# Kernel optimization log

Hardware: AMD Instinct MI355X
Metric: run time of the kernel (lower is better)

The kernel has to match this reference:

```python
import jax, jax.numpy as jnp
import numpy as np

KERNEL_MUL = 2.0
KERNEL_NUM = 5

def setup_inputs() -> dict:
    key = jax.random.key(0)
    k1, k2 = jax.random.split(key)
    source = jax.random.normal(k1, (4096, 256), dtype=jnp.float32)
    target = jax.random.normal(k2, (4096, 256), dtype=jnp.float32)
    return {"source": source, "target": target}

def reference(source, target):
    B = source.shape[0]
    total = jnp.concatenate([source, target], axis=0)           # [2N, D]
    n = total.shape[0]
    # pairwise squared L2 distances via expansion (same math as
    # ((total0 - total1)**2).sum(2) without the [2N,2N,D] intermediate)
    sq = jnp.sum(total * total, axis=-1)                         # [2N]
    l2 = jnp.maximum(sq[:, None] + sq[None, :] - 2.0 * (total @ total.T), 0.0)  # [2N,2N]
    # bandwidth from data mean of off-diagonal distances (detached in torch via .data)
    bandwidth = jax.lax.stop_gradient(jnp.sum(l2)) / (n * n - n)
    bandwidth = bandwidth / (KERNEL_MUL ** (KERNEL_NUM // 2))
    kernels = jnp.zeros_like(l2)
    for i in range(KERNEL_NUM):
        kernels = kernels + jnp.exp(-l2 / (bandwidth * (KERNEL_MUL ** i)))
    xx = kernels[:B, :B]
    yy = kernels[B:, B:]
    xy = kernels[:B, B:]
    yx = kernels[B:, :B]
    return jnp.mean(xx + yy - xy - yx)
```

## Files before the change

kernel.cpp:

```cpp
#include <hip/hip_runtime.h>


#define NROWS 8192
#define BHALF 4096
#define DDIM  256
#define TILE  128
#define NTILE 64
#define NBLK  2080

typedef __attribute__((ext_vector_type(8))) short bf16x8;
typedef __attribute__((ext_vector_type(4))) float f32x4;
typedef __attribute__((ext_vector_type(2))) float f32x2;
typedef __attribute__((ext_vector_type(4))) unsigned short u16x4;

struct Ws {
  float coef;
  float Spart[256];
  float cpart[256][256];
  float sq[NROWS];
  float part[NBLK];
};

__device__ __forceinline__ unsigned short f2bf(float x) {
  unsigned int u = __builtin_bit_cast(unsigned int, x);
  return (unsigned short)((u + 0x7fffu + ((u >> 16) & 1u)) >> 16);
}

__device__ __forceinline__ const float* row_ptr(const float* src, const float* tgt, int i) {
  return (i < BHALF) ? (src + (size_t)i * DDIM) : (tgt + (size_t)(i - BHALF) * DDIM);
}

__global__ __launch_bounds__(256) void k_prep(const float* __restrict__ src,
                                              const float* __restrict__ tgt,
                                              Ws* __restrict__ ws,
                                              unsigned short* __restrict__ tb,
                                              int conv) {
  __shared__ float cls[4][256];
  __shared__ float sred[4];
  int tid = threadIdx.x, wave = tid >> 6, lane = tid & 63;
  int row0 = blockIdx.x * 32 + wave * 8;
  float c0 = 0.f, c1 = 0.f, c2 = 0.f, c3 = 0.f;
  float s[8];
  #pragma unroll
  for (int r = 0; r < 8; ++r) {
    const float4* rp = (const float4*)row_ptr(src, tgt, row0 + r);
    float4 x = rp[lane];
    if (conv) {
      u16x4 b = { f2bf(x.x), f2bf(x.y), f2bf(x.z), f2bf(x.w) };
      int rg = row0 + r;
      int t = rg >> 7, rl = rg & 127;
      int cg = lane >> 1;
      int kc = cg >> 3, cwp = cg & 7;
      int slot = cwp ^ (rl & 7);
      *(u16x4*)&tb[((size_t)(t * 4 + kc) * 128 + rl) * 64 + slot * 8 + (lane & 1) * 4] = b;
    }
    c0 += x.x; c1 += x.y; c2 += x.z; c3 += x.w;
    s[r] = x.x * x.x + x.y * x.y + x.z * x.z + x.w * x.w;
  }
  #pragma unroll
  for (int off = 32; off > 0; off >>= 1) {
    #pragma unroll
    for (int r = 0; r < 8; ++r) s[r] += __shfl_xor(s[r], off);
  }
  if (lane == 0) {
    float Sw = 0.f;
    #pragma unroll
    for (int r = 0; r < 8; ++r) { ws->sq[row0 + r] = s[r]; Sw += s[r]; }
    sred[wave] = Sw;
  }
  cls[wave][lane * 4 + 0] = c0;
  cls[wave][lane * 4 + 1] = c1;
  cls[wave][lane * 4 + 2] = c2;
  cls[wave][lane * 4 + 3] = c3;
  __syncthreads();
  ws->cpart[blockIdx.x][tid] = cls[0][tid] + cls[1][tid] + cls[2][tid] + cls[3][tid];
  if (tid == 0) ws->Spart[blockIdx.x] = sred[0] + sred[1] + sred[2] + sred[3];
}

__global__ __launch_bounds__(256) void k_bw(Ws* __restrict__ ws) {
  __shared__ float redm[4], reds[4];
  int tid = threadIdx.x, wave = tid >> 6, lane = tid & 63;
  float mc = 0.f;
  for (int b0 = 0; b0 < 256; b0 += 16) {
    float v[16];
    #pragma unroll
    for (int j = 0; j < 16; ++j) v[j] = ws->cpart[b0 + j][tid];
    #pragma unroll
    for (int j = 0; j < 16; ++j) mc += v[j];
  }
  float p = mc * mc;
  float sp = ws->Spart[tid];
  #pragma unroll
  for (int off = 32; off > 0; off >>= 1) {
    p  += __shfl_xor(p, off);
    sp += __shfl_xor(sp, off);
  }
  if (lane == 0) { redm[wave] = p; reds[wave] = sp; }
  __syncthreads();
  if (tid == 0) {
    float msq = redm[0] + redm[1] + redm[2] + redm[3];
    float S   = reds[0] + reds[1] + reds[2] + reds[3];
    double n = (double)NROWS;
    double sum_l2 = 2.0 * n * (double)S - 2.0 * (double)msq;
    double bw = sum_l2 / (n * n - n) / 4.0;
    ws->coef = (float)(1.4426950408889634 / (16.0 * bw));
  }
}

__device__ __forceinline__ void stage_tiles(const unsigned short* gA,
                                            const unsigned short* gB,
                                            unsigned short* lA, unsigned short* lB,
                                            int kc) {
  #pragma unroll
  for (int t = 0; t < 4; ++t) {
    __builtin_amdgcn_global_load_lds(
        (const __attribute__((address_space(1))) void*)(gA + (size_t)kc * 8192 + t * 512),
        (__attribute__((address_space(3))) void*)(lA + t * 512), 16, 0, 0);
    __builtin_amdgcn_global_load_lds(
        (const __attribute__((address_space(1))) void*)(gB + (size_t)kc * 8192 + t * 512),
        (__attribute__((address_space(3))) void*)(lB + t * 512), 16, 0, 0);
  }
}

template <int FAST>
__global__ __launch_bounds__(256, 4) void k_main(const unsigned short* __restrict__ tb,
                                                 const float* __restrict__ src,
                                                 const float* __restrict__ tgt,
                                                 Ws* __restrict__ ws) {
  int bid = blockIdx.x;
  int idx = (bid & 7) * (NBLK / 8) + (bid >> 3);
  int ti = (int)((129.0 - sqrt(129.0 * 129.0 - 8.0 * (double)idx)) * 0.5);
  while (64 * (ti + 1) - ((ti + 1) * ti) / 2 <= idx) ++ti;
  while (64 * ti - (ti * (ti - 1)) / 2 > idx) --ti;
  int tj = ti + (idx - (64 * ti - (ti * (ti - 1)) / 2));

  __shared__ __align__(16) unsigned short As[TILE * 64];
  __shared__ __align__(16) unsigned short Bs[TILE * 64];
  __shared__ float wsum[4];

  int tid = threadIdx.x;
  int wave = tid >> 6, lane = tid & 63;
  int wm = wave >> 1, wn = wave & 1;
  int lr = lane & 15, q = lane >> 4;
  int Ib = ti * TILE, Jb = tj * TILE;

  f32x4 zero = {0.f, 0.f, 0.f, 0.f};
  f32x4 acc[4][4];
  #pragma unroll
  for (int m = 0; m < 4; ++m)
    #pragma unroll
    for (int n = 0; n < 4; ++n) acc[m][n] = zero;

  const unsigned short* gA = nullptr; const unsigned short* gB = nullptr;
  if (FAST) {
    gA = tb + (size_t)ti * 4 * 8192 + wave * 2048 + lane * 8;
    gB = tb + (size_t)tj * 4 * 8192 + wave * 2048 + lane * 8;
  }
  int r0 = tid >> 4, c4 = tid & 15;

  #pragma unroll
  for (int kc = 0; kc < 4; ++kc) {
    if (kc) __syncthreads();
    if (FAST) {
      stage_tiles(gA, gB, &As[(wave * 32) * 64], &Bs[(wave * 32) * 64], kc);
    } else {
      #pragma unroll
      for (int rr = 0; rr < 8; ++rr) {
        int row = rr * 16 + r0;
        int sw = ((c4 >> 1) ^ (row & 7)) * 8 + (c4 & 1) * 4;
        float4 va = ((const float4*)row_ptr(src, tgt, Ib + row))[kc * 16 + c4];
        u16x4 ba = { f2bf(va.x), f2bf(va.y), f2bf(va.z), f2bf(va.w) };
        *(u16x4*)&As[row * 64 + sw] = ba;
        float4 vb = ((const float4*)row_ptr(src, tgt, Jb + row))[kc * 16 + c4];
        u16x4 bb = { f2bf(vb.x), f2bf(vb.y), f2bf(vb.z), f2bf(vb.w) };
        *(u16x4*)&Bs[row * 64 + sw] = bb;
      }
    }
    __syncthreads();
    #pragma unroll
    for (int kk = 0; kk < 2; ++kk) {
      int cidx = ((kk * 4 + q) ^ (lr & 7)) << 3;
      bf16x8 af[4], bfr[4];
      #pragma unroll
      for (int m = 0; m < 4; ++m)
        af[m] = *(const bf16x8*)&As[(wm * 64 + m * 16 + lr) * 64 + cidx];
      #pragma unroll
      for (int n = 0; n < 4; ++n)
        bfr[n] = *(const bf16x8*)&Bs[(wn * 64 + n * 16 + lr) * 64 + cidx];
      #pragma unroll
      for (int m = 0; m < 4; ++m)
        #pragma unroll
        for (int n = 0; n < 4; ++n)
          acc[m][n] = __builtin_amdgcn_mfma_f32_16x16x32_bf16(af[m], bfr[n], acc[m][n], 0, 0, 0);
    }
  }

  float coef = ws->coef;
  float coef2 = 2.f * coef;
  int ibase = Ib + wm * 64;
  int jbase = Jb + wn * 64;
  float nscj[4];
  f32x2 nsci01[4], nsci23[4];
  #pragma unroll
  for (int n = 0; n < 4; ++n) nscj[n] = -ws->sq[jbase + n * 16 + lr] * coef;
  #pragma unroll
  for (int m = 0; m < 4; ++m) {
    nsci01[m] = f32x2{ -ws->sq[ibase + m * 16 + q * 4 + 0] * coef,
                       -ws->sq[ibase + m * 16 + q * 4 + 1] * coef };
    nsci23[m] = f32x2{ -ws->sq[ibase + m * 16 + q * 4 + 2] * coef,
                       -ws->sq[ibase + m * 16 + q * 4 + 3] * coef };
  }

  const f32x2 c2v = { coef2, coef2 };
  f32x2 accA = {0.f, 0.f}, accB = {0.f, 0.f};
  f32x2 accC = {0.f, 0.f}, accD = {0.f, 0.f};
  #pragma unroll
  for (int m = 0; m < 4; ++m) {
    #pragma unroll
    for (int n = 0; n < 4; ++n) {
      f32x4 g = acc[m][n];
      f32x2 bj = { nscj[n], nscj[n] };
      f32x2 b01 = nsci01[m] + bj;
      f32x2 b23 = nsci23[m] + bj;
      f32x2 a01 = f32x2{g[0], g[1]} * c2v + b01;
      f32x2 a23 = f32x2{g[2], g[3]} * c2v + b23;
      f32x2 t0, t1;
      t0.x = __builtin_amdgcn_exp2f(a01.x); t0.y = __builtin_amdgcn_exp2f(a01.y);
      t1.x = __builtin_amdgcn_exp2f(a23.x); t1.y = __builtin_amdgcn_exp2f(a23.y);
      f32x2 p0 = t0 * t0, p1 = t1 * t1;
      f32x2 q0 = p0 * p0, q1 = p1 * p1;
      f32x2 r0v = q0 * q0, r1v = q1 * q1;
      accA += t0 + p0;
      accB += q0 + r0v;
      accA = r0v * r0v + accA;
      accC += t1 + p1;
      accD += q1 + r1v;
      accC = r1v * r1v + accC;
    }
  }
  float lsum = (accA.x + accA.y) + (accB.x + accB.y)
             + (accC.x + accC.y) + (accD.x + accD.y);
  #pragma unroll
  for (int off = 32; off > 0; off >>= 1) lsum += __shfl_xor(lsum, off);
  if (lane == 0) wsum[wave] = lsum;
  __syncthreads();
  if (tid == 0) {
    float tot = wsum[0] + wsum[1] + wsum[2] + wsum[3];
    float sA = (ti < 32) ? 1.f : -1.f;
    float sB = (tj < 32) ? 1.f : -1.f;
    float fac = sA * sB * ((ti == tj) ? 1.f : 2.f);
    ws->part[blockIdx.x] = fac * tot;
  }
}

__global__ __launch_bounds__(256) void k_final(const Ws* __restrict__ ws,
                                               float* __restrict__ out) {
  __shared__ double red[4];
  int tid = threadIdx.x, wave = tid >> 6, lane = tid & 63;
  double s = 0.0;
  for (int i = tid; i < NBLK; i += 256) s += (double)ws->part[i];
  #pragma unroll
  for (int off = 32; off > 0; off >>= 1) s += __shfl_xor(s, off);
  if (lane == 0) red[wave] = s;
  __syncthreads();
  if (tid == 0)
    out[0] = (float)((red[0] + red[1] + red[2] + red[3]) /
                     ((double)BHALF * (double)BHALF));
}

extern "C" void kernel_launch(void* const* d_in, const int* in_sizes, int n_in,
                              void* d_out, int out_size, void* d_ws, size_t ws_size,
                              hipStream_t stream) {
  const float* src = (const float*)d_in[0];
  const float* tgt = (const float*)d_in[1];
  Ws* ws = (Ws*)d_ws;
  float* out = (float*)d_out;

  size_t wsoff = (sizeof(Ws) + 255) & ~(size_t)255;
  size_t need = wsoff + (size_t)NROWS * DDIM * 2;
  bool fast = ws_size >= need;
  unsigned short* tb = fast ? (unsigned short*)((char*)d_ws + wsoff) : nullptr;

  hipLaunchKernelGGL(k_prep, dim3(256), dim3(256), 0, stream, src, tgt, ws, tb,
                     fast ? 1 : 0);
  hipLaunchKernelGGL(k_bw, dim3(1), dim3(256), 0, stream, ws);
  if (fast)
    hipLaunchKernelGGL((k_main<1>), dim3(NBLK), dim3(256), 0, stream, tb, src, tgt, ws);
  else
    hipLaunchKernelGGL((k_main<0>), dim3(NBLK), dim3(256), 0, stream, tb, src, tgt, ws);
  hipLaunchKernelGGL(k_final, dim3(1), dim3(256), 0, stream, ws, out);
}
```

Before: 100.0 us.

## Make k_main persistent over multiple tiles and prefetch next tile during epilogue

```diff
diff --git a/kernel.cpp b/kernel.cpp
--- a/kernel.cpp
+++ b/kernel.cpp
@@ -7,6 +7,7 @@
 #define TILE  128
 #define NTILE 64
 #define NBLK  2080
+#define NPER  1024
 
 typedef __attribute__((ext_vector_type(8))) short bf16x8;
 typedef __attribute__((ext_vector_type(4))) float f32x4;
@@ -28,6 +29,14 @@
 
 __device__ __forceinline__ const float* row_ptr(const float* src, const float* tgt, int i) {
   return (i < BHALF) ? (src + (size_t)i * DDIM) : (tgt + (size_t)(i - BHALF) * DDIM);
+}
+
+__device__ __forceinline__ void derive_tile(int idx, int& ti_o, int& tj_o) {
+  int t = (int)((129.0 - sqrt(129.0 * 129.0 - 8.0 * (double)idx)) * 0.5);
+  while (64 * (t + 1) - ((t + 1) * t) / 2 <= idx) ++t;
+  while (64 * t - (t * (t - 1)) / 2 > idx) --t;
+  ti_o = t;
+  tj_o = t + (idx - (64 * t - (t * (t - 1)) / 2));
 }
 
 __global__ __launch_bounds__(256) void k_prep(const float* __restrict__ src,
@@ -127,12 +136,10 @@
                                                  const float* __restrict__ src,
                                                  const float* __restrict__ tgt,
                                                  Ws* __restrict__ ws) {
-  int bid = blockIdx.x;
-  int idx = (bid & 7) * (NBLK / 8) + (bid >> 3);
-  int ti = (int)((129.0 - sqrt(129.0 * 129.0 - 8.0 * (double)idx)) * 0.5);
-  while (64 * (ti + 1) - ((ti + 1) * ti) / 2 <= idx) ++ti;
-  while (64 * ti - (ti * (ti - 1)) / 2 > idx) --ti;
-  int tj = ti + (idx - (64 * ti - (ti * (ti - 1)) / 2));
+  int b = blockIdx.x;
+  int c = b & 7, p = b >> 3;
+  int nw = (p < 4) ? 3 : 2;
+  int idx = c * 260 + p;
 
   __shared__ __align__(16) unsigned short As[TILE * 64];
   __shared__ __align__(16) unsigned short Bs[TILE * 64];
@@ -142,114 +149,161 @@
   int wave = tid >> 6, lane = tid & 63;
   int wm = wave >> 1, wn = wave & 1;
   int lr = lane & 15, q = lane >> 4;
-  int Ib = ti * TILE, Jb = tj * TILE;
-
-  f32x4 zero = {0.f, 0.f, 0.f, 0.f};
-  f32x4 acc[4][4];
-  #pragma unroll
-  for (int m = 0; m < 4; ++m)
-    #pragma unroll
-    for (int n = 0; n < 4; ++n) acc[m][n] = zero;
-
+
+  int ti, tj;
+  derive_tile(idx, ti, tj);
+
+  unsigned short* lA = &As[(wave * 32) * 64];
+  unsigned short* lB = &Bs[(wave * 32) * 64];
   const unsigned short* gA = nullptr; const unsigned short* gB = nullptr;
   if (FAST) {
-    gA = tb + (size_t)ti * 4 * 8192 + wave * 2048 + lane * 8;
-    gB = tb + (size_t)tj * 4 * 8192 + wave * 2048 + lane * 8;
+    gA = tb + (size_t)ti * 32768 + wave * 2048 + lane * 8;
+    gB = tb + (size_t)tj * 32768 + wave * 2048 + lane * 8;
+    stage_tiles(gA, gB, lA, lB, 0);
   }
   int r0 = tid >> 4, c4 = tid & 15;
-
-  #pragma unroll
-  for (int kc = 0; kc < 4; ++kc) {
-    if (kc) __syncthreads();
-    if (FAST) {
-      stage_tiles(gA, gB, &As[(wave * 32) * 64], &Bs[(wave * 32) * 64], kc);
-    } else {
-      #pragma unroll
-      for (int rr = 0; rr < 8; ++rr) {
-        int row = rr * 16 + r0;
-        int sw = ((c4 >> 1) ^ (row & 7)) * 8 + (c4 & 1) * 4;
-        float4 va = ((const float4*)row_ptr(src, tgt, Ib + row))[kc * 16 + c4];
-        u16x4 ba = { f2bf(va.x), f2bf(va.y), f2bf(va.z), f2bf(va.w) };
-        *(u16x4*)&As[row * 64 + sw] = ba;
-        float4 vb = ((const float4*)row_ptr(src, tgt, Jb + row))[kc * 16 + c4];
-        u16x4 bb = { f2bf(vb.x), f2bf(vb.y), f2bf(vb.z), f2bf(vb.w) };
-        *(u16x4*)&Bs[row * 64 + sw] = bb;
-      }
-    }
-    __syncthreads();
-    #pragma unroll
-    for (int kk = 0; kk < 2; ++kk) {
-      int cidx = ((kk * 4 + q) ^ (lr & 7)) << 3;
-      bf16x8 af[4], bfr[4];
-      #pragma unroll
-      for (int m = 0; m < 4; ++m)
-        af[m] = *(const bf16x8*)&As[(wm * 64 + m * 16 + lr) * 64 + cidx];
-      #pragma unroll
-      for (int n = 0; n < 4; ++n)
-        bfr[n] = *(const bf16x8*)&Bs[(wn * 64 + n * 16 + lr) * 64 + cidx];
-      #pragma unroll
-      for (int m = 0; m < 4; ++m)
-        #pragma unroll
-        for (int n = 0; n < 4; ++n)
-          acc[m][n] = __builtin_amdgcn_mfma_f32_16x16x32_bf16(af[m], bfr[n], acc[m][n], 0, 0, 0);
-    }
-  }
-
   float coef = ws->coef;
   float coef2 = 2.f * coef;
-  int ibase = Ib + wm * 64;
-  int jbase = Jb + wn * 64;
-  float nscj[4];
-  f32x2 nsci01[4], nsci23[4];
-  #pragma unroll
-  for (int n = 0; n < 4; ++n) nscj[n] = -ws->sq[jbase + n * 16 + lr] * coef;
-  #pragma unroll
-  for (int m = 0; m < 4; ++m) {
-    nsci01[m] = f32x2{ -ws->sq[ibase + m * 16 + q * 4 + 0] * coef,
-                       -ws->sq[ibase + m * 16 + q * 4 + 1] * coef };
-    nsci23[m] = f32x2{ -ws->sq[ibase + m * 16 + q * 4 + 2] * coef,
-                       -ws->sq[ibase + m * 16 + q * 4 + 3] * coef };
-  }
-
   const f32x2 c2v = { coef2, coef2 };
-  f32x2 accA = {0.f, 0.f}, accB = {0.f, 0.f};
-  f32x2 accC = {0.f, 0.f}, accD = {0.f, 0.f};
-  #pragma unroll
-  for (int m = 0; m < 4; ++m) {
-    #pragma unroll
-    for (int n = 0; n < 4; ++n) {
-      f32x4 g = acc[m][n];
-      f32x2 bj = { nscj[n], nscj[n] };
-      f32x2 b01 = nsci01[m] + bj;
-      f32x2 b23 = nsci23[m] + bj;
-      f32x2 a01 = f32x2{g[0], g[1]} * c2v + b01;
-      f32x2 a23 = f32x2{g[2], g[3]} * c2v + b23;
-      f32x2 t0, t1;
-      t0.x = __builtin_amdgcn_exp2f(a01.x); t0.y = __builtin_amdgcn_exp2f(a01.y);
-      t1.x = __builtin_amdgcn_exp2f(a23.x); t1.y = __builtin_amdgcn_exp2f(a23.y);
-      f32x2 p0 = t0 * t0, p1 = t1 * t1;
-      f32x2 q0 = p0 * p0, q1 = p1 * p1;
-      f32x2 r0v = q0 * q0, r1v = q1 * q1;
-      accA += t0 + p0;
-      accB += q0 + r0v;
-      accA = r0v * r0v + accA;
-      accC += t1 + p1;
-      accD += q1 + r1v;
-      accC = r1v * r1v + accC;
-    }
-  }
-  float lsum = (accA.x + accA.y) + (accB.x + accB.y)
-             + (accC.x + accC.y) + (accD.x + accD.y);
-  #pragma unroll
-  for (int off = 32; off > 0; off >>= 1) lsum += __shfl_xor(lsum, off);
-  if (lane == 0) wsum[wave] = lsum;
-  __syncthreads();
-  if (tid == 0) {
-    float tot = wsum[0] + wsum[1] + wsum[2] + wsum[3];
-    float sA = (ti < 32) ? 1.f : -1.f;
-    float sB = (tj < 32) ? 1.f : -1.f;
-    float fac = sA * sB * ((ti == tj) ? 1.f : 2.f);
-    ws->part[blockIdx.x] = fac * tot;
+  const int coffbase = 0;
+  (void)coffbase;
+
+  for (int w = 0; w < nw; ++w) {
+    f32x4 zero = {0.f, 0.f, 0.f, 0.f};
+    f32x4 acc[4][4];
+    #pragma unroll
+    for (int m = 0; m < 4; ++m)
+      #pragma unroll
+      for (int n = 0; n < 4; ++n) acc[m][n] = zero;
+
+    if (FAST) {
+      if (w == 0) __syncthreads();
+      #pragma unroll
+      for (int kc = 0; kc < 4; ++kc) {
+        if (kc) {
+          __syncthreads();
+          stage_tiles(gA, gB, lA, lB, kc);
+          __syncthreads();
+        }
+        #pragma unroll
+        for (int kk = 0; kk < 2; ++kk) {
+          int cidx = ((kk * 4 + q) ^ (lr & 7)) << 3;
+          bf16x8 af[4], bfr[4];
+          #pragma unroll
+          for (int m = 0; m < 4; ++m)
+            af[m] = *(const bf16x8*)&As[(wm * 64 + m * 16 + lr) * 64 + cidx];
+          #pragma unroll
+          for (int n = 0; n < 4; ++n)
+            bfr[n] = *(const bf16x8*)&Bs[(wn * 64 + n * 16 + lr) * 64 + cidx];
+          #pragma unroll
+          for (int m = 0; m < 4; ++m)
+            #pragma unroll
+            for (int n = 0; n < 4; ++n)
+              acc[m][n] = __builtin_amdgcn_mfma_f32_16x16x32_bf16(af[m], bfr[n], acc[m][n], 0, 0, 0);
+        }
+      }
+      __syncthreads();
+    } else {
+      int Ib = ti * TILE, Jb = tj * TILE;
+      #pragma unroll
+      for (int kc = 0; kc < 4; ++kc) {
+        if (kc || w) __syncthreads();
+        #pragma unroll
+        for (int rr = 0; rr < 8; ++rr) {
+          int row = rr * 16 + r0;
+          int sw = ((c4 >> 1) ^ (row & 7)) * 8 + (c4 & 1) * 4;
+          float4 va = ((const float4*)row_ptr(src, tgt, Ib + row))[kc * 16 + c4];
+          u16x4 ba = { f2bf(va.x), f2bf(va.y), f2bf(va.z), f2bf(va.w) };
+          *(u16x4*)&As[row * 64 + sw] = ba;
+          float4 vb = ((const float4*)row_ptr(src, tgt, Jb + row))[kc * 16 + c4];
+          u16x4 bb = { f2bf(vb.x), f2bf(vb.y), f2bf(vb.z), f2bf(vb.w) };
+          *(u16x4*)&Bs[row * 64 + sw] = bb;
+        }
+        __syncthreads();
+        #pragma unroll
+        for (int kk = 0; kk < 2; ++kk) {
+          int cidx = ((kk * 4 + q) ^ (lr & 7)) << 3;
+          bf16x8 af[4], bfr[4];
+          #pragma unroll
+          for (int m = 0; m < 4; ++m)
+            af[m] = *(const bf16x8*)&As[(wm * 64 + m * 16 + lr) * 64 + cidx];
+          #pragma unroll
+          for (int n = 0; n < 4; ++n)
+            bfr[n] = *(const bf16x8*)&Bs[(wn * 64 + n * 16 + lr) * 64 + cidx];
+          #pragma unroll
+          for (int m = 0; m < 4; ++m)
+            #pragma unroll
+            for (int n = 0; n < 4; ++n)
+              acc[m][n] = __builtin_amdgcn_mfma_f32_16x16x32_bf16(af[m], bfr[n], acc[m][n], 0, 0, 0);
+        }
+      }
+    }
+
+    int eti = ti, etj = tj, eidx = idx;
+    bool more = (w + 1 < nw);
+    if (more) {
+      idx += 128;
+      derive_tile(idx, ti, tj);
+      if (FAST) {
+        gA = tb + (size_t)ti * 32768 + wave * 2048 + lane * 8;
+        gB = tb + (size_t)tj * 32768 + wave * 2048 + lane * 8;
+        stage_tiles(gA, gB, lA, lB, 0);
+      }
+    }
+
+    int ibase = eti * TILE + wm * 64;
+    int jbase = etj * TILE + wn * 64;
+    float nscj[4];
+    f32x2 nsci01[4], nsci23[4];
+    #pragma unroll
+    for (int n = 0; n < 4; ++n) nscj[n] = -ws->sq[jbase + n * 16 + lr] * coef;
+    #pragma unroll
+    for (int m = 0; m < 4; ++m) {
+      nsci01[m] = f32x2{ -ws->sq[ibase + m * 16 + q * 4 + 0] * coef,
+                         -ws->sq[ibase + m * 16 + q * 4 + 1] * coef };
+      nsci23[m] = f32x2{ -ws->sq[ibase + m * 16 + q * 4 + 2] * coef,
+                         -ws->sq[ibase + m * 16 + q * 4 + 3] * coef };
+    }
+    f32x2 accA = {0.f, 0.f}, accB = {0.f, 0.f};
+    f32x2 accC = {0.f, 0.f}, accD = {0.f, 0.f};
+    #pragma unroll
+    for (int m = 0; m < 4; ++m) {
+      #pragma unroll
+      for (int n = 0; n < 4; ++n) {
+        f32x4 g = acc[m][n];
+        f32x2 bj = { nscj[n], nscj[n] };
+        f32x2 b01 = nsci01[m] + bj;
+        f32x2 b23 = nsci23[m] + bj;
+        f32x2 a01 = f32x2{g[0], g[1]} * c2v + b01;
+        f32x2 a23 = f32x2{g[2], g[3]} * c2v + b23;
+        f32x2 t0, t1;
+        t0.x = __builtin_amdgcn_exp2f(a01.x); t0.y = __builtin_amdgcn_exp2f(a01.y);
+        t1.x = __builtin_amdgcn_exp2f(a23.x); t1.y = __builtin_amdgcn_exp2f(a23.y);
+        f32x2 p0 = t0 * t0, p1 = t1 * t1;
+        f32x2 q0 = p0 * p0, q1 = p1 * p1;
+        f32x2 r0v = q0 * q0, r1v = q1 * q1;
+        accA += t0 + p0;
+        accB += q0 + r0v;
+        accA = r0v * r0v + accA;
+        accC += t1 + p1;
+        accD += q1 + r1v;
+        accC = r1v * r1v + accC;
+      }
+    }
+    float lsum = (accA.x + accA.y) + (accB.x + accB.y)
+               + (accC.x + accC.y) + (accD.x + accD.y);
+    #pragma unroll
+    for (int off = 32; off > 0; off >>= 1) lsum += __shfl_xor(lsum, off);
+    if (lane == 0) wsum[wave] = lsum;
+    __syncthreads();
+    if (tid == 0) {
+      float tot = wsum[0] + wsum[1] + wsum[2] + wsum[3];
+      float sA = (eti < 32) ? 1.f : -1.f;
+      float sB = (etj < 32) ? 1.f : -1.f;
+      float fac = sA * sB * ((eti == etj) ? 1.f : 2.f);
+      int slot = (eidx % 260) * 8 + eidx / 260;
+      ws->part[slot] = fac * tot;
+    }
   }
 }
 
@@ -285,8 +339,8 @@
                      fast ? 1 : 0);
   hipLaunchKernelGGL(k_bw, dim3(1), dim3(256), 0, stream, ws);
   if (fast)
-    hipLaunchKernelGGL((k_main<1>), dim3(NBLK), dim3(256), 0, stream, tb, src, tgt, ws);
+    hipLaunchKernelGGL((k_main<1>), dim3(NPER), dim3(256), 0, stream, tb, src, tgt, ws);
   else
-    hipLaunchKernelGGL((k_main<0>), dim3(NBLK), dim3(256), 0, stream, tb, src, tgt, ws);
+    hipLaunchKernelGGL((k_main<0>), dim3(NPER), dim3(256), 0, stream, tb, src, tgt, ws);
   hipLaunchKernelGGL(k_final, dim3(1), dim3(256), 0, stream, ws, out);
 }
```

New measurement: 101.3 us. About the same (+1.3%).
